# Performance work log

Hardware: AMD Instinct MI355X
Metric: run time of the kernel (lower is better)

Reference implementation:

```python
import jax, jax.numpy as jnp
import numpy as np

B = 262144
N_MAX = 4
N_EXPERTS = sum(n * n for n in range(1, N_MAX + 1))  # 30
# offset of expert block for each n (experts within n indexed by l*l + l + m)
OFFSETS = np.cumsum([0] + [n * n for n in range(1, N_MAX)])  # [0,1,5,14]


def _expert_id(n, l, m):
    off = jnp.asarray(OFFSETS, dtype=jnp.int32)
    return off[n - 1] + l * l + l + m  # (B,) int


def setup_inputs() -> dict:
    key = jax.random.key(0)
    ks = jax.random.split(key, 12)
    x = jax.random.normal(ks[0], (B, 3), dtype=jnp.float32)
    # valid coupled quantum numbers: 1<=n<=4, 0<=l<n, -l<=m<=l
    n = jax.random.randint(ks[1], (B,), 1, N_MAX + 1)
    ul = jax.random.uniform(ks[2], (B,))
    l = jnp.floor(ul * n.astype(jnp.float32)).astype(jnp.int32)
    l = jnp.clip(l, 0, n - 1)
    um = jax.random.uniform(ks[3], (B,))
    m = jnp.floor(um * (2 * l + 1).astype(jnp.float32)).astype(jnp.int32) - l
    m = jnp.clip(m, -l, l)
    s = 0.1
    W0 = jax.random.normal(ks[4], (3, 128), dtype=jnp.float32) * s
    b0 = jnp.zeros((128,), dtype=jnp.float32)
    W1 = jax.random.normal(ks[5], (128, 64), dtype=jnp.float32) * s
    b1 = jnp.zeros((64,), dtype=jnp.float32)
    Wa = jax.random.normal(ks[6], (N_EXPERTS, 64, 32), dtype=jnp.float32) * s
    ba = jax.random.normal(ks[7], (N_EXPERTS, 32), dtype=jnp.float32) * s
    Wb = jax.random.normal(ks[8], (N_EXPERTS, 32, 2), dtype=jnp.float32) * s
    bb = jax.random.normal(ks[9], (N_EXPERTS, 2), dtype=jnp.float32) * s
    return {"x": x, "n": n.astype(jnp.int32), "l": l, "m": m,
            "W0": W0, "b0": b0, "W1": W1, "b1": b1,
            "Wa": Wa, "ba": ba, "Wb": Wb, "bb": bb}


def reference(x, n, l, m, W0, b0, W1, b1, Wa, ba, Wb, bb):
    eid = _expert_id(n, l, m)  # (B,)
    # shared trunk (dropout is identity in eval mode)
    h = jnp.tanh(x @ W0 + b0)          # (B,128)
    h = jnp.tanh(h @ W1 + b1)          # (B,64)
    # per-sample expert dispatch via irregular gather of tiny MLP weights
    g = jnp.tanh(jnp.einsum('bd,bdh->bh', h, Wa[eid]) + ba[eid])  # (B,32)
    psi = jnp.einsum('bh,bho->bo', g, Wb[eid]) + bb[eid]          # (B,2)
    norm = jnp.sqrt(jnp.sum(psi * psi, axis=1, keepdims=True) + 1e-6)
    return psi / norm
```

## Files before the change

### kernel.cpp

```cpp
#include <hip/hip_runtime.h>
#include <math.h>


#define THREADS 64
#define NE 30
#define HB 256
#define PER 1024
#define ETS 16
#define MAXBLK 4126
#define SA 67
#define SG 36

typedef short bf16x8 __attribute__((ext_vector_type(8)));
typedef float f32x4 __attribute__((ext_vector_type(4)));

__device__ __forceinline__ int expert_id(int nn, int ll, int mm) {
    return ((nn - 1) * nn * (2 * nn - 1)) / 6 + ll * ll + ll + mm;
}

__device__ __forceinline__ float fast_tanh(float v) {
    float e = __builtin_exp2f(v * 2.885390082f);
    return fmaf(-2.0f, __builtin_amdgcn_rcpf(e + 1.0f), 1.0f);
}

__device__ __forceinline__ unsigned int f2b(float f) {
    unsigned int u = __float_as_uint(f);
    return (u + 0x7fffu + ((u >> 16) & 1u)) >> 16;
}
__device__ __forceinline__ float b2f(unsigned int b) {
    return __uint_as_float(b << 16);
}
__device__ __forceinline__ unsigned int packsplit(float v) {
    const unsigned int hb = f2b(v);
    const float lo = v - b2f(hb);
    return (__float_as_uint(lo) & 0xffff0000u) | hb;
}

union U8 { unsigned int u[4]; bf16x8 v; };
__device__ __forceinline__ void unpack8(const unsigned int* w, bf16x8& hi, bf16x8& lo) {
    U8 H, L;
#pragma unroll
    for (int i = 0; i < 4; ++i) {
        H.u[i] = __builtin_amdgcn_perm(w[2 * i + 1], w[2 * i], 0x05040100u);
        L.u[i] = __builtin_amdgcn_perm(w[2 * i + 1], w[2 * i], 0x07060302u);
    }
    hi = H.v; lo = L.v;
}

__global__ void hist_pack_kernel(const int* __restrict__ nq, const int* __restrict__ lq,
                                 const int* __restrict__ mq,
                                 int* __restrict__ eids, int* __restrict__ etot,
                                 int* __restrict__ bbase,
                                 const float* __restrict__ W1,
                                 unsigned short* __restrict__ W1fh, unsigned short* __restrict__ W1fl,
                                 const float* __restrict__ Wa,
                                 unsigned short* __restrict__ Wafh, unsigned short* __restrict__ Wafl,
                                 int B) {
    const int tid = threadIdx.x;
    const int bx = blockIdx.x;
    if (bx < HB) {
        __shared__ int h[NE];
        if (tid < NE) h[tid] = 0;
        __syncthreads();
        const int base = bx * PER;
        for (int i = tid; i < PER; i += blockDim.x) {
            const int e = expert_id(nq[base + i], lq[base + i], mq[base + i]);
            eids[base + i] = e;
            atomicAdd(&h[e], 1);
        }
        __syncthreads();
        if (tid < NE)
            bbase[bx * NE + tid] = atomicAdd(&etot[tid * ETS], h[tid]);
    } else if (bx == HB) {
        for (int i = tid; i < 8192; i += blockDim.x) {
            const int j = i & 7, s = (i >> 3) & 15, q = (i >> 7) & 3;
            const int nt = (i >> 9) & 3, c = i >> 11;
            const int k = c * 32 + q * 8 + j, n = nt * 16 + s;
            const float w = W1[k * 64 + n];
            const unsigned int hb = f2b(w);
            W1fh[i] = (unsigned short)hb;
            W1fl[i] = (unsigned short)f2b(w - b2f(hb));
        }
    } else {
        const int e = bx - HB - 1;
        for (int i = tid; i < 2048; i += blockDim.x) {
            const int j = i & 7, s = (i >> 3) & 15, q = (i >> 7) & 3;
            const int nt2 = (i >> 9) & 1, c2 = (i >> 10) & 1;
            const int d = c2 * 32 + q * 8 + j, hh = nt2 * 16 + s;
            const float w = Wa[e * 2048 + d * 32 + hh];
            const unsigned int hb = f2b(w);
            Wafh[e * 2048 + i] = (unsigned short)hb;
            Wafl[e * 2048 + i] = (unsigned short)f2b(w - b2f(hb));
        }
    }
}

__global__ void scatter_kernel(const int* __restrict__ eids, const int* __restrict__ etot,
                               const int* __restrict__ bbase, int* __restrict__ perm,
                               int4* __restrict__ desc, int B) {
    const int tid = threadIdx.x;
    if (blockIdx.x == HB) {
        __shared__ int tq[NE], es[NE], pb[NE + 1];
        if (tid < NE) tq[tid] = etot[tid * ETS];
        __syncthreads();
        if (tid == 0) {
            int e0 = 0, c = 0;
            for (int e = 0; e < NE; ++e) {
                es[e] = e0; pb[e] = c;
                c += (tq[e] + THREADS - 1) >> 6;
                e0 += tq[e];
            }
            pb[NE] = c;
        }
        __syncthreads();
        const int tot = pb[NE];
        for (int b = tid; b < MAXBLK; b += blockDim.x) {
            int4 d = make_int4(-1, 0, 0, 0);
            if (b < tot) {
                int e = 0;
                while (pb[e + 1] <= b) ++e;
                const int seg = b - pb[e];
                d.x = e;
                d.y = es[e] + (seg << 6);
                d.z = min(THREADS, tq[e] - (seg << 6));
            }
            desc[b] = d;
        }
        return;
    }
    __shared__ int lcnt[NE], esrt[NE], bb[NE], tq[NE];
    if (tid < NE) {
        lcnt[tid] = 0;
        bb[tid] = bbase[blockIdx.x * NE + tid];
        tq[tid] = etot[tid * ETS];
    }
    __syncthreads();
    if (tid == 0) {
        int es0 = 0;
        for (int e = 0; e < NE; ++e) { esrt[e] = es0; es0 += tq[e]; }
    }
    __syncthreads();
    const int blk = blockIdx.x * PER;
    for (int i = tid; i < PER; i += blockDim.x) {
        const int idx = blk + i;
        const int e = eids[idx];
        const int r = atomicAdd(&lcnt[e], 1);
        perm[esrt[e] + bb[e] + r] = idx;
    }
}

__global__ __launch_bounds__(THREADS, 4) void wfc_kernel(
    const float* __restrict__ x, const int* __restrict__ perm,
    const int4* __restrict__ desc,
    const float* __restrict__ W0, const float* __restrict__ b0,
    const bf16x8* __restrict__ W1fh, const bf16x8* __restrict__ W1fl,
    const float* __restrict__ b1,
    const bf16x8* __restrict__ Wafh, const bf16x8* __restrict__ Wafl,
    const float* __restrict__ ba,
    const float* __restrict__ Wb, const float* __restrict__ bb,
    float* __restrict__ out)
{
    __shared__ unsigned int sbuf[2304];

    const int4 dsc = desc[blockIdx.x];
    if (dsc.x < 0) return;
    const int eid  = __builtin_amdgcn_readfirstlane(dsc.x);
    const int start = dsc.y;
    const int cnt   = dsc.z;

    const int tid = threadIdx.x;
    const bool valid = tid < cnt;
    const int idx = perm[start + (valid ? tid : 0)];

    const int lane = tid & 63;
    const int wv   = tid >> 6;
    const int qd   = lane >> 4;
    const int l16  = lane & 15;

    const float x0 = x[idx * 3 + 0];
    const float x1 = x[idx * 3 + 1];
    const float x2 = x[idx * 3 + 2];

    f32x4 acc[4][4];
#pragma unroll
    for (int nt = 0; nt < 4; ++nt) {
        const float bv = b1[nt * 16 + l16];
#pragma unroll
        for (int mt = 0; mt < 4; ++mt) {
            f32x4 c; c[0] = bv; c[1] = bv; c[2] = bv; c[3] = bv;
            acc[mt][nt] = c;
        }
    }

    for (int c = 0; c < 4; ++c) {
        if (c) __syncthreads();
#pragma unroll
        for (int kk = 0; kk < 32; ++kk) {
            const int k = c * 32 + kk;
            const float pre = fmaf(x0, W0[k], fmaf(x1, W0[128 + k], fmaf(x2, W0[256 + k], b0[k])));
            sbuf[kk * SA + tid] = packsplit(fast_tanh(pre));
        }
        __syncthreads();

        bf16x8 Bhi[4], Blo[4];
#pragma unroll
        for (int nt = 0; nt < 4; ++nt) {
            const int rec = (c * 4 + nt) * 64 + qd * 16 + l16;
            Bhi[nt] = W1fh[rec];
            Blo[nt] = W1fl[rec];
        }
#pragma unroll
        for (int mt = 0; mt < 4; ++mt) {
            unsigned int a[8];
            const int mrow = wv * 64 + mt * 16 + l16;
#pragma unroll
            for (int j = 0; j < 8; ++j) a[j] = sbuf[(qd * 8 + j) * SA + mrow];
            bf16x8 Ahi, Alo;
            unpack8(a, Ahi, Alo);
#pragma unroll
            for (int nt = 0; nt < 4; ++nt) {
                acc[mt][nt] = __builtin_amdgcn_mfma_f32_16x16x32_bf16(Ahi, Bhi[nt], acc[mt][nt], 0, 0, 0);
                acc[mt][nt] = __builtin_amdgcn_mfma_f32_16x16x32_bf16(Ahi, Blo[nt], acc[mt][nt], 0, 0, 0);
                acc[mt][nt] = __builtin_amdgcn_mfma_f32_16x16x32_bf16(Alo, Bhi[nt], acc[mt][nt], 0, 0, 0);
            }
        }
    }

    f32x4 acc2[4][2];
#pragma unroll
    for (int nt2 = 0; nt2 < 2; ++nt2) {
        const float bv = ba[(eid << 5) + nt2 * 16 + l16];
#pragma unroll
        for (int mt = 0; mt < 4; ++mt) {
            f32x4 c; c[0] = bv; c[1] = bv; c[2] = bv; c[3] = bv;
            acc2[mt][nt2] = c;
        }
    }

    const bf16x8* __restrict__ waeh = Wafh + (eid << 8);
    const bf16x8* __restrict__ wael = Wafl + (eid << 8);
    for (int c2 = 0; c2 < 2; ++c2) {
        __syncthreads();
#pragma unroll
        for (int mt = 0; mt < 4; ++mt) {
#pragma unroll
            for (int ntl = 0; ntl < 2; ++ntl) {
#pragma unroll
                for (int r = 0; r < 4; ++r) {
                    const float h2 = fast_tanh(acc[mt][c2 * 2 + ntl][r]);
                    const int dl  = ntl * 16 + l16;
                    const int row = wv * 64 + mt * 16 + qd * 4 + r;
                    sbuf[dl * SA + row] = packsplit(h2);
                }
            }
        }
        __syncthreads();

        bf16x8 B2hi[2], B2lo[2];
#pragma unroll
        for (int nt2 = 0; nt2 < 2; ++nt2) {
            const int rec = (c2 * 2 + nt2) * 64 + qd * 16 + l16;
            B2hi[nt2] = waeh[rec];
            B2lo[nt2] = wael[rec];
        }
#pragma unroll
        for (int mt = 0; mt < 4; ++mt) {
            unsigned int a[8];
            const int mrow = wv * 64 + mt * 16 + l16;
#pragma unroll
            for (int j = 0; j < 8; ++j) a[j] = sbuf[(qd * 8 + j) * SA + mrow];
            bf16x8 Ahi, Alo;
            unpack8(a, Ahi, Alo);
#pragma unroll
            for (int nt2 = 0; nt2 < 2; ++nt2) {
                acc2[mt][nt2] = __builtin_amdgcn_mfma_f32_16x16x32_bf16(Ahi, B2hi[nt2], acc2[mt][nt2], 0, 0, 0);
                acc2[mt][nt2] = __builtin_amdgcn_mfma_f32_16x16x32_bf16(Ahi, B2lo[nt2], acc2[mt][nt2], 0, 0, 0);
                acc2[mt][nt2] = __builtin_amdgcn_mfma_f32_16x16x32_bf16(Alo, B2hi[nt2], acc2[mt][nt2], 0, 0, 0);
            }
        }
    }

    __syncthreads();
    float* g2 = (float*)sbuf;
#pragma unroll
    for (int mt = 0; mt < 4; ++mt) {
#pragma unroll
        for (int nt2 = 0; nt2 < 2; ++nt2) {
#pragma unroll
            for (int r = 0; r < 4; ++r) {
                const int row = wv * 64 + mt * 16 + qd * 4 + r;
                g2[row * SG + nt2 * 16 + l16] = fast_tanh(acc2[mt][nt2][r]);
            }
        }
    }
    __syncthreads();

    float gv[32];
    {
        const float4* grow = (const float4*)(g2 + tid * SG);
#pragma unroll
        for (int i = 0; i < 8; ++i) {
            float4 v = grow[i];
            gv[4 * i + 0] = v.x; gv[4 * i + 1] = v.y;
            gv[4 * i + 2] = v.z; gv[4 * i + 3] = v.w;
        }
    }

    const float* __restrict__ wbe = Wb + (eid << 6);
    float p0 = bb[2 * eid], p1 = bb[2 * eid + 1];
#pragma unroll
    for (int h = 0; h < 32; ++h) {
        p0 = fmaf(gv[h], wbe[2 * h + 0], p0);
        p1 = fmaf(gv[h], wbe[2 * h + 1], p1);
    }

    const float s = fmaf(p0, p0, fmaf(p1, p1, 1e-6f));
    const float inv = 1.0f / sqrtf(s);
    if (valid) {
        float2 o; o.x = p0 * inv; o.y = p1 * inv;
        ((float2*)out)[idx] = o;
    }
}

extern "C" void kernel_launch(void* const* d_in, const int* in_sizes, int n_in,
                              void* d_out, int out_size, void* d_ws, size_t ws_size,
                              hipStream_t stream) {
    const float* x  = (const float*)d_in[0];
    const int*   n  = (const int*)d_in[1];
    const int*   l  = (const int*)d_in[2];
    const int*   m  = (const int*)d_in[3];
    const float* W0 = (const float*)d_in[4];
    const float* b0 = (const float*)d_in[5];
    const float* W1 = (const float*)d_in[6];
    const float* b1 = (const float*)d_in[7];
    const float* Wa = (const float*)d_in[8];
    const float* ba = (const float*)d_in[9];
    const float* Wb = (const float*)d_in[10];
    const float* bb = (const float*)d_in[11];
    float* out = (float*)d_out;

    const int B = in_sizes[1];

    int*            perm  = (int*)d_ws;
    int*            eids  = perm + B;
    int*            bbase = eids + B;
    int*            etot  = bbase + HB * NE;
    int4*           desc  = (int4*)(etot + 512);
    unsigned short* W1fh  = (unsigned short*)(desc + MAXBLK);
    unsigned short* W1fl  = W1fh + 8192;
    unsigned short* Wafh  = W1fl + 8192;
    unsigned short* Wafl  = Wafh + NE * 2048;

    hipMemsetAsync(etot, 0, NE * ETS * sizeof(int), stream);
    hist_pack_kernel<<<HB + 1 + NE, 256, 0, stream>>>(
        n, l, m, eids, etot, bbase, W1, W1fh, W1fl, Wa, Wafh, Wafl, B);
    scatter_kernel<<<HB + 1, 256, 0, stream>>>(eids, etot, bbase, perm, desc, B);
    wfc_kernel<<<MAXBLK, THREADS, 0, stream>>>(
        x, perm, desc, W0, b0,
        (const bf16x8*)W1fh, (const bf16x8*)W1fl, b1,
        (const bf16x8*)Wafh, (const bf16x8*)Wafl, ba, Wb, bb, out);
}
```

Baseline: 147.0 us.

## Replace global atomic histogram with per-block counts and in-kernel prefix sums

The histogram kernel now records each sample's local rank together with its expert id and writes per-block counts, with no global atomics. The scatter kernel loads all block counts into shared memory and computes each block's base offset and the expert totals itself. This removes the memset launch, the global atomic contention and the second round of shared atomics during scatter. In exchange, every scatter block redundantly reads and scans the full 256x30 count table, about 30 KB of shared memory per block.

```diff
diff --git a/kernel.cpp b/kernel.cpp
--- a/kernel.cpp
+++ b/kernel.cpp
@@ -6,7 +6,6 @@
 #define NE 30
 #define HB 256
 #define PER 1024
-#define ETS 16
 #define MAXBLK 4126
 #define SA 67
 #define SG 36
@@ -49,8 +48,7 @@
 
 __global__ void hist_pack_kernel(const int* __restrict__ nq, const int* __restrict__ lq,
                                  const int* __restrict__ mq,
-                                 int* __restrict__ eids, int* __restrict__ etot,
-                                 int* __restrict__ bbase,
+                                 int* __restrict__ eidr, int* __restrict__ cnt,
                                  const float* __restrict__ W1,
                                  unsigned short* __restrict__ W1fh, unsigned short* __restrict__ W1fl,
                                  const float* __restrict__ Wa,
@@ -65,12 +63,11 @@
         const int base = bx * PER;
         for (int i = tid; i < PER; i += blockDim.x) {
             const int e = expert_id(nq[base + i], lq[base + i], mq[base + i]);
-            eids[base + i] = e;
-            atomicAdd(&h[e], 1);
-        }
-        __syncthreads();
-        if (tid < NE)
-            bbase[bx * NE + tid] = atomicAdd(&etot[tid * ETS], h[tid]);
+            const int r = atomicAdd(&h[e], 1);
+            eidr[base + i] = (r << 5) | e;
+        }
+        __syncthreads();
+        if (tid < NE) cnt[bx * NE + tid] = h[tid];
     } else if (bx == HB) {
         for (int i = tid; i < 8192; i += blockDim.x) {
             const int j = i & 7, s = (i >> 3) & 15, q = (i >> 7) & 3;
@@ -95,21 +92,37 @@
     }
 }
 
-__global__ void scatter_kernel(const int* __restrict__ eids, const int* __restrict__ etot,
-                               const int* __restrict__ bbase, int* __restrict__ perm,
-                               int4* __restrict__ desc, int B) {
+__global__ void scatter_kernel(const int* __restrict__ eidr, const int* __restrict__ cnt,
+                               int* __restrict__ perm, int4* __restrict__ desc) {
+    __shared__ int cl[HB * NE];
+    __shared__ int bb[NE], tq[NE], esrt[NE + 1];
     const int tid = threadIdx.x;
-    if (blockIdx.x == HB) {
-        __shared__ int tq[NE], es[NE], pb[NE + 1];
-        if (tid < NE) tq[tid] = etot[tid * ETS];
-        __syncthreads();
+    const int bx = blockIdx.x;
+    for (int i = tid; i < HB * NE; i += blockDim.x) cl[i] = cnt[i];
+    __syncthreads();
+    if (tid < NE) {
+        int s = 0, mybase = 0;
+#pragma unroll 4
+        for (int blk = 0; blk < HB; ++blk) {
+            if (blk == bx) mybase = s;
+            s += cl[blk * NE + tid];
+        }
+        bb[tid] = mybase;
+        tq[tid] = s;
+    }
+    __syncthreads();
+    if (tid == 0) {
+        int es = 0;
+        for (int e = 0; e < NE; ++e) { esrt[e] = es; es += tq[e]; }
+        esrt[NE] = es;
+    }
+    __syncthreads();
+
+    if (bx == HB) {
+        __shared__ int pb[NE + 1];
         if (tid == 0) {
-            int e0 = 0, c = 0;
-            for (int e = 0; e < NE; ++e) {
-                es[e] = e0; pb[e] = c;
-                c += (tq[e] + THREADS - 1) >> 6;
-                e0 += tq[e];
-            }
+            int c = 0;
+            for (int e = 0; e < NE; ++e) { pb[e] = c; c += (tq[e] + THREADS - 1) >> 6; }
             pb[NE] = c;
         }
         __syncthreads();
@@ -121,31 +134,19 @@
                 while (pb[e + 1] <= b) ++e;
                 const int seg = b - pb[e];
                 d.x = e;
-                d.y = es[e] + (seg << 6);
+                d.y = esrt[e] + (seg << 6);
                 d.z = min(THREADS, tq[e] - (seg << 6));
             }
             desc[b] = d;
         }
         return;
     }
-    __shared__ int lcnt[NE], esrt[NE], bb[NE], tq[NE];
-    if (tid < NE) {
-        lcnt[tid] = 0;
-        bb[tid] = bbase[blockIdx.x * NE + tid];
-        tq[tid] = etot[tid * ETS];
-    }
-    __syncthreads();
-    if (tid == 0) {
-        int es0 = 0;
-        for (int e = 0; e < NE; ++e) { esrt[e] = es0; es0 += tq[e]; }
-    }
-    __syncthreads();
-    const int blk = blockIdx.x * PER;
+
+    const int base = bx * PER;
     for (int i = tid; i < PER; i += blockDim.x) {
-        const int idx = blk + i;
-        const int e = eids[idx];
-        const int r = atomicAdd(&lcnt[e], 1);
-        perm[esrt[e] + bb[e] + r] = idx;
+        const int p = eidr[base + i];
+        const int e = p & 31;
+        perm[esrt[e] + bb[e] + (p >> 5)] = base + i;
     }
 }
 
@@ -342,19 +343,17 @@
     const int B = in_sizes[1];
 
     int*            perm  = (int*)d_ws;
-    int*            eids  = perm + B;
-    int*            bbase = eids + B;
-    int*            etot  = bbase + HB * NE;
-    int4*           desc  = (int4*)(etot + 512);
+    int*            eidr  = perm + B;
+    int*            cnt   = eidr + B;
+    int4*           desc  = (int4*)(cnt + HB * NE);
     unsigned short* W1fh  = (unsigned short*)(desc + MAXBLK);
     unsigned short* W1fl  = W1fh + 8192;
     unsigned short* Wafh  = W1fl + 8192;
     unsigned short* Wafl  = Wafh + NE * 2048;
 
-    hipMemsetAsync(etot, 0, NE * ETS * sizeof(int), stream);
     hist_pack_kernel<<<HB + 1 + NE, 256, 0, stream>>>(
-        n, l, m, eids, etot, bbase, W1, W1fh, W1fl, Wa, Wafh, Wafl, B);
-    scatter_kernel<<<HB + 1, 256, 0, stream>>>(eids, etot, bbase, perm, desc, B);
+        n, l, m, eidr, cnt, W1, W1fh, W1fl, Wa, Wafh, Wafl, B);
+    scatter_kernel<<<HB + 1, 256, 0, stream>>>(eidr, cnt, perm, desc);
     wfc_kernel<<<MAXBLK, THREADS, 0, stream>>>(
         x, perm, desc, W0, b0,
         (const bf16x8*)W1fh, (const bf16x8*)W1fl, b1,
```

After: 156.8 us. 6.6% more time.
